# Optimization experiments

Hardware: AMD Instinct MI355X
Metric: run time of the kernel (lower is better)

The kernel has to match this reference:

```python
import jax, jax.numpy as jnp
import numpy as np

K_KNN = 20
TC = 3  # taylor_channel
N_TERMS = 20  # trivariate polynomial terms up to order 3
CHANNELS = [(6, 32), (32, 64), (64, 128), (128, 256)]


def _knn_indices(xyz, k):
    sq = jnp.sum(xyz * xyz, axis=1)  # B x N
    d2 = sq[:, :, None] + sq[:, None, :] - 2.0 * jnp.einsum('bci,bcj->bij', xyz, xyz)
    _, idx = jax.lax.top_k(-d2, k)
    return idx


def _group(feat, idx):
    # feat: B x C x N, idx: B x N x K -> B x C x N x K
    return jax.vmap(lambda f, i: f[:, i])(feat, idx)


def _taylor_terms(g):
    X, Y, Z = g[:, 0], g[:, 1], g[:, 2]
    one = jnp.ones_like(X)
    terms = [one, X, Y, Z, X * Y, X * Z, Y * Z, X * X, Y * Y, Z * Z,
             X * X * Y, X * X * Z, X * Y * Y, Y * Y * Z, X * Z * Z, Y * Z * Z,
             X * Y * Z, X * X * X, Y * Y * Y, Z * Z * Z]
    return jnp.stack(terms, axis=1)


def _spider_conv(feat, idx, terms, w1, b1, w2, b2):
    # feat: B x C x N; w1: tc x 20; w2: out x (C*tc) x K
    B, C, N = feat.shape
    g = _group(feat, idx)  # B x C x N x K
    taylor = jnp.einsum('btnk,ot->bonk', terms, w1) + b1[None, :, None, None]
    g = (g[:, :, None, :, :] * taylor[:, None, :, :, :]).reshape(B, C * TC, N, g.shape[-1])
    out = jnp.einsum('bcnk,ock->bon', g, w2) + b2[None, :, None]
    return jax.nn.relu(out)


def _forward(pc, params):
    # pc: B x N x 6
    pcT = jnp.transpose(pc, (0, 2, 1))
    xyz = pcT[:, 0:3, :]
    idx = _knn_indices(xyz, K_KNN)  # B x N x K
    grouped_xyz = _group(xyz, idx)
    grouped_pc = grouped_xyz - xyz[:, :, :, None]  # relative coords
    terms = _taylor_terms(grouped_pc)
    feat = pcT
    feats = []
    for l in range(4):
        w1, b1, w2, b2 = params[l]
        feat = _spider_conv(feat, idx, terms, w1, b1, w2, b2)
        feats.append(feat)
    cat = jnp.concatenate(feats, axis=1)
    top2, _ = jax.lax.top_k(cat, 2)  # topk over point dim (last axis)
    return top2.reshape(cat.shape[0], -1)  # B x 960


def setup_inputs() -> dict:
    key = jax.random.key(0)
    keys = jax.random.split(key, 1 + 16)
    B, N = 4, 2048
    inp = {'pc': jax.random.normal(keys[0], (B, N, 6), dtype=jnp.float32)}
    ki = 1
    for l, (cin, cout) in enumerate(CHANNELS):
        inp[f'w1_{l}'] = jax.random.normal(keys[ki], (TC, N_TERMS), dtype=jnp.float32) * 0.1; ki += 1
        inp[f'b1_{l}'] = jax.random.normal(keys[ki], (TC,), dtype=jnp.float32) * 0.01; ki += 1
        inp[f'w2_{l}'] = jax.random.normal(keys[ki], (cout, cin * TC, K_KNN), dtype=jnp.float32) * (1.0 / np.sqrt(cin * TC * K_KNN)); ki += 1
        inp[f'b2_{l}'] = jax.random.normal(keys[ki], (cout,), dtype=jnp.float32) * 0.01; ki += 1
    return inp


def reference(pc, w1_0, b1_0, w2_0, b2_0, w1_1, b1_1, w2_1, b2_1,
              w1_2, b1_2, w2_2, b2_2, w1_3, b1_3, w2_3, b2_3):
    params = [(w1_0, b1_0, w2_0, b2_0), (w1_1, b1_1, w2_1, b2_1),
              (w1_2, b1_2, w2_2, b2_2), (w1_3, b1_3, w2_3, b2_3)]
    return _forward(pc, params)
```

## Files before the change

kernel.cpp:

```cpp
#include <hip/hip_runtime.h>
#include <math.h>

#define BB 4
#define NN 2048
#define KNN 20

typedef _Float16 f16x8 __attribute__((ext_vector_type(8)));
typedef _Float16 f16x4 __attribute__((ext_vector_type(4)));
typedef _Float16 f16x2 __attribute__((ext_vector_type(2)));
typedef float f32x4 __attribute__((ext_vector_type(4)));

#define DPP_STEP(CTRL, RMASK)                                                   \
    {                                                                           \
        unsigned ov = (unsigned)__builtin_amdgcn_update_dpp(                    \
            (int)bv, (int)bv, CTRL, RMASK, 0xf, false);                         \
        unsigned oj = (unsigned)__builtin_amdgcn_update_dpp(                    \
            (int)jj, (int)jj, CTRL, RMASK, 0xf, false);                         \
        bool lt = (ov < bv) || (ov == bv && oj < jj);                           \
        bv = lt ? ov : bv;                                                      \
        jj = lt ? oj : jj;                                                      \
    }

__global__ __launch_bounds__(256) void knn_kernel(const float* __restrict__ pc,
                                                  int* __restrict__ idx_out,
                                                  float* __restrict__ rel_out) {
    __shared__ float4 sp[NN];
    const int tid = threadIdx.x;
    const int b = blockIdx.x / (NN / 4);
    const int grp = blockIdx.x % (NN / 4);
    for (int p = tid; p < NN; p += 256) {
        float x = pc[(size_t)(b * NN + p) * 6 + 0];
        float y = pc[(size_t)(b * NN + p) * 6 + 1];
        float z = pc[(size_t)(b * NN + p) * 6 + 2];
        float4 v;
        v.x = x; v.y = y; v.z = z;
        v.w = __fadd_rn(__fadd_rn(__fmul_rn(x, x), __fmul_rn(y, y)), __fmul_rn(z, z));
        sp[p] = v;
    }
    __syncthreads();
    const int lane = tid & 63;
    const int i = grp * 4 + (tid >> 6);
    const float4 pi = sp[i];
    const float xi = pi.x, yi = pi.y, zi = pi.z, sqi = pi.w;

    unsigned mmr[32];
#pragma unroll
    for (int t = 0; t < 32; ++t) {
        const int j = t * 64 + lane;
        const float4 pj = sp[j];
        float dot = __fadd_rn(__fadd_rn(__fmul_rn(xi, pj.x), __fmul_rn(yi, pj.y)),
                              __fmul_rn(zi, pj.z));
        float d2 = __fsub_rn(__fadd_rn(sqi, pj.w), __fmul_rn(2.0f, dot));
        unsigned bbits = __float_as_uint(d2);
        mmr[t] = bbits ^ (0x80000000u | (unsigned)((int)bbits >> 31));
    }

    const unsigned UMAX = 0xFFFFFFFFu;
    unsigned mask = 0u;
    unsigned v1, t1, v2, t2;

    auto refill = [&]() {
        v1 = UMAX; t1 = 0u; v2 = UMAX; t2 = 0u;
#pragma unroll
        for (int t = 0; t < 32; ++t) {
            unsigned m = ((mask >> t) & 1u) ? UMAX : mmr[t];
            bool c1 = m < v1;
            bool c2 = m < v2;
            unsigned nv2 = c1 ? v1 : (c2 ? m : v2);
            unsigned nt2 = c1 ? t1 : (c2 ? (unsigned)t : t2);
            v1 = c1 ? m : v1;
            t1 = c1 ? (unsigned)t : t1;
            v2 = nv2; t2 = nt2;
        }
    };
    refill();

    const size_t orow = (size_t)(b * NN + i);
    for (int k = 0; k < KNN; ++k) {
        unsigned bv = v1;
        unsigned jj = (t1 << 6) | (unsigned)lane;
        DPP_STEP(0x111, 0xf)
        DPP_STEP(0x112, 0xf)
        DPP_STEP(0x114, 0xf)
        DPP_STEP(0x118, 0xf)
        DPP_STEP(0x142, 0xa)
        DPP_STEP(0x143, 0xc)
        const unsigned sj = (unsigned)__builtin_amdgcn_readlane((int)jj, 63);
        if (lane == 0) {
            idx_out[orow * KNN + k] = (int)sj;
            const float4 pj = sp[sj];
            size_t ro = (orow * KNN + k) * 3;
            rel_out[ro + 0] = __fsub_rn(pj.x, xi);
            rel_out[ro + 1] = __fsub_rn(pj.y, yi);
            rel_out[ro + 2] = __fsub_rn(pj.z, zi);
        }
        if (k < KNN - 1) {
            bool am = ((sj & 63u) == (unsigned)lane);
            if (am) {
                mask |= (1u << (sj >> 6));
                v1 = v2; t1 = t2; v2 = UMAX;
            }
            if (__ballot(v1 == UMAX) != 0ull) refill();
        }
    }
}

__global__ __launch_bounds__(256) void taylor_all_kernel(
    const float* __restrict__ rel,
    const float* __restrict__ w10, const float* __restrict__ b10, _Float16* __restrict__ ty0,
    const float* __restrict__ w11, const float* __restrict__ b11, _Float16* __restrict__ ty1,
    const float* __restrict__ w12, const float* __restrict__ b12, _Float16* __restrict__ ty2,
    const float* __restrict__ w13, const float* __restrict__ b13, _Float16* __restrict__ ty3) {
    __shared__ float w1s[4][60];
    __shared__ float b1s[4][3];
    const int tid = threadIdx.x;
    if (tid < 240) {
        const float* wp = (tid < 60) ? w10 : (tid < 120) ? w11 : (tid < 180) ? w12 : w13;
        w1s[tid / 60][tid % 60] = wp[tid % 60];
    } else if (tid < 252) {
        int r = tid - 240;
        const float* bp = (r < 3) ? b10 : (r < 6) ? b11 : (r < 9) ? b12 : b13;
        b1s[r / 3][r % 3] = bp[r % 3];
    }
    __syncthreads();
    int t = blockIdx.x * 256 + tid;
    if (t >= BB * NN * KNN) return;
    float X = rel[(size_t)t * 3 + 0], Y = rel[(size_t)t * 3 + 1], Z = rel[(size_t)t * 3 + 2];
    float tm[20];
    tm[0] = 1.f; tm[1] = X; tm[2] = Y; tm[3] = Z;
    tm[4] = X * Y; tm[5] = X * Z; tm[6] = Y * Z;
    tm[7] = X * X; tm[8] = Y * Y; tm[9] = Z * Z;
    tm[10] = X * X * Y; tm[11] = X * X * Z; tm[12] = X * Y * Y; tm[13] = Y * Y * Z;
    tm[14] = X * Z * Z; tm[15] = Y * Z * Z; tm[16] = X * Y * Z;
    tm[17] = X * X * X; tm[18] = Y * Y * Y; tm[19] = Z * Z * Z;
    _Float16* typ[4] = {ty0, ty1, ty2, ty3};
#pragma unroll
    for (int l = 0; l < 4; ++l) {
#pragma unroll
        for (int o = 0; o < 3; ++o) {
            float a = b1s[l][o];
#pragma unroll
            for (int q = 0; q < 20; ++q) a += w1s[l][o * 20 + q] * tm[q];
            typ[l][(size_t)t * 3 + o] = (_Float16)a;
        }
    }
}

struct WsplitArgs {
    const float* w2[4];
    _Float16* wf[4];
    int COUT[4], CIN[4], CPAD[4], OCB[4], KCB[4];
    int cum[4];
};

__global__ __launch_bounds__(256) void wsplit_all_kernel(WsplitArgs a) {
    int e = blockIdx.x * 256 + threadIdx.x;
    if (e >= a.cum[3]) return;
    int l = (e >= a.cum[0]) + (e >= a.cum[1]) + (e >= a.cum[2]);
    int base = l ? a.cum[l - 1] : 0;
    e -= base;
    const int KCB = a.KCB[l], OCB = a.OCB[l], CPAD = a.CPAD[l], CIN = a.CIN[l];
    int i = e & 7;
    int lane = (e >> 3) & 63;
    int fi = e >> 9;
    int kcb = fi % KCB;
    int ocb = (fi / KCB) % OCB;
    int k = fi / (KCB * OCB);
    int oc = ocb * 16 + (lane & 15);
    int kk = kcb * 32 + (lane >> 4) * 8 + i;
    int o = kk / CPAD, c = kk % CPAD;
    float x = 0.f;
    if (o < 3 && c < CIN)
        x = a.w2[l][((size_t)oc * (CIN * 3) + c * 3 + o) * KNN + k];
    a.wf[l][e] = (_Float16)x;
}

template <int CIN, int COUT, int CK3P, int NT, int WM, int WN, int FM, int FN,
          int OCT, int KSPLIT, bool L0S, bool F16IN>
__global__ __launch_bounds__(256) void convm_kernel(const void* __restrict__ fin,
                                                    const int* __restrict__ idx,
                                                    const _Float16* __restrict__ tyg,
                                                    const _Float16* __restrict__ wf,
                                                    float* __restrict__ out) {
    constexpr int KR = KNN / KSPLIT;
    constexpr int SR = CK3P + 8;
    constexpr int KCB = CK3P / 32;
    constexpr int OCB = COUT / 16;
    constexpr int OCBLK = WM * FM * 16;
    constexpr int NTL = NN / NT;
    constexpr int TPR = 256 / NT;
    constexpr int CT = L0S ? 6 : (CIN / TPR);
    constexpr int CQ = L0S ? 2 : (CT >= 4 ? CT / 4 : 1);
    constexpr int GF = (CT >= 8) ? CT / 8 : 1;
    static_assert(WN * FN * 16 == NT, "n tiling");
    static_assert(OCBLK * OCT == COUT, "oc tiling");
    static_assert(WM * WN == 4, "4 waves");

    __shared__ _Float16 Bs[NT * SR];
    __shared__ _Float16 tyt[NT][3 * KR];
    __shared__ int idxt[NT][KR];

    const float* finf = (const float*)fin;
    const _Float16* finh = (const _Float16*)fin;

    const int tid = threadIdx.x;
    const int lane = tid & 63;
    const int wid = tid >> 6;
    const int wm = wid / WN;
    const int wn = wid % WN;
    int t = blockIdx.x;
    const int b = t % BB;      t /= BB;
    const int ks = t % KSPLIT; t /= KSPLIT;
    const int oct = t % OCT;   t /= OCT;
    const int ntl = t;
    const int n0 = ntl * NT;
    const int oc0 = oct * OCBLK;
    const int k0 = ks * KR;
    const size_t brow = (size_t)b * NN;

    for (int e = tid; e < NT * KR; e += 256) {
        int n = e / KR, kk = e % KR;
        idxt[n][kk] = idx[(brow + n0 + n) * KNN + k0 + kk];
    }
    for (int e = tid; e < NT * 3 * KR; e += 256) {
        int n = e / (3 * KR), q = e % (3 * KR);
        tyt[n][q] = tyg[((brow + n0 + n) * KNN + k0) * 3 + q];
    }
    __syncthreads();

    const int nrow = tid % NT;
    const int sub = tid / NT;
    float4 g[CQ];
    f16x8 gf[GF];

    auto issue_gather = [&](int kk) {
        if constexpr (L0S) {
            if (tid < 192) {
                int j = idxt[nrow][kk];
                const float* p = finf + (brow + j) * 6;
                g[0] = *reinterpret_cast<const float4*>(p);
                float2 r2 = *reinterpret_cast<const float2*>(p + 4);
                g[1].x = r2.x; g[1].y = r2.y;
            }
        } else if constexpr (F16IN) {
            int j = idxt[nrow][kk];
            const _Float16* p = finh + (brow + j) * CIN + sub * CT;
#pragma unroll
            for (int q = 0; q < GF; ++q)
                gf[q] = *reinterpret_cast<const f16x8*>(p + q * 8);
        } else {
            int j = idxt[nrow][kk];
            const float* p = finf + (brow + j) * CIN + sub * CT;
#pragma unroll
            for (int q = 0; q < CQ; ++q)
                g[q] = *reinterpret_cast<const float4*>(p + q * 4);
        }
    };
    issue_gather(0);

    f32x4 acc[FM][FN];
#pragma unroll
    for (int fm = 0; fm < FM; ++fm)
#pragma unroll
        for (int fn = 0; fn < FN; ++fn) acc[fm][fn] = (f32x4){0.f, 0.f, 0.f, 0.f};

    f16x8 areg[FM * KCB];
    auto loadA_burst = [&](int k) {
#pragma unroll
        for (int fm = 0; fm < FM; ++fm)
#pragma unroll
            for (int kcb = 0; kcb < KCB; ++kcb) {
                size_t fidx = ((size_t)k * OCB + (oc0 >> 4) + wm * FM + fm) * KCB + kcb;
                areg[fm * KCB + kcb] =
                    *reinterpret_cast<const f16x8*>(&wf[(fidx * 64 + lane) * 8]);
            }
    };

    for (int kk = 0; kk < KR; ++kk) {
        const int k = k0 + kk;
        loadA_burst(k);
        __syncthreads();
        if constexpr (L0S) {
            if (tid < 192) {
                _Float16 th = tyt[nrow][kk * 3 + sub];
                f16x2 tb; tb[0] = th; tb[1] = th;
                f16x2 g0, g1, g2;
                g0[0] = (_Float16)g[0].x; g0[1] = (_Float16)g[0].y;
                g1[0] = (_Float16)g[0].z; g1[1] = (_Float16)g[0].w;
                g2[0] = (_Float16)g[1].x; g2[1] = (_Float16)g[1].y;
                f16x2 p0 = g0 * tb, p1 = g1 * tb, p2 = g2 * tb;
                f16x8 hv;
                hv[0] = p0[0]; hv[1] = p0[1]; hv[2] = p1[0]; hv[3] = p1[1];
                hv[4] = p2[0]; hv[5] = p2[1]; hv[6] = (_Float16)0.f; hv[7] = (_Float16)0.f;
                *reinterpret_cast<f16x8*>(&Bs[nrow * SR + sub * 8]) = hv;
                if (sub == 0) {
                    f16x8 z = {};
                    *reinterpret_cast<f16x8*>(&Bs[nrow * SR + 24]) = z;
                }
            }
        } else {
            f16x2 gh[CT / 2];
            if constexpr (F16IN) {
                const f16x2* gp = reinterpret_cast<const f16x2*>(gf);
#pragma unroll
                for (int q = 0; q < CT / 2; ++q) gh[q] = gp[q];
            } else {
#pragma unroll
                for (int q = 0; q < CQ; ++q) {
                    f16x2 a0, a1;
                    a0[0] = (_Float16)g[q].x; a0[1] = (_Float16)g[q].y;
                    a1[0] = (_Float16)g[q].z; a1[1] = (_Float16)g[q].w;
                    gh[2 * q] = a0; gh[2 * q + 1] = a1;
                }
            }
            _Float16 th0 = tyt[nrow][kk * 3 + 0];
            _Float16 th1 = tyt[nrow][kk * 3 + 1];
            _Float16 th2 = tyt[nrow][kk * 3 + 2];
#pragma unroll
            for (int o = 0; o < 3; ++o) {
                _Float16 th = (o == 0) ? th0 : (o == 1) ? th1 : th2;
                f16x2 tb; tb[0] = th; tb[1] = th;
#pragma unroll
                for (int qp = 0; qp < CT / 8; ++qp) {
                    f16x2 p0 = gh[4 * qp + 0] * tb;
                    f16x2 p1 = gh[4 * qp + 1] * tb;
                    f16x2 p2 = gh[4 * qp + 2] * tb;
                    f16x2 p3 = gh[4 * qp + 3] * tb;
                    f16x8 hv;
                    hv[0] = p0[0]; hv[1] = p0[1]; hv[2] = p1[0]; hv[3] = p1[1];
                    hv[4] = p2[0]; hv[5] = p2[1]; hv[6] = p3[0]; hv[7] = p3[1];
                    *reinterpret_cast<f16x8*>(
                        &Bs[nrow * SR + o * CIN + sub * CT + qp * 8]) = hv;
                }
            }
        }
        __syncthreads();
        if (kk + 1 < KR) issue_gather(kk + 1);
#pragma unroll
        for (int kcb = 0; kcb < KCB; ++kcb) {
            f16x8 bf[FN];
#pragma unroll
            for (int fn = 0; fn < FN; ++fn) {
                int row = wn * FN * 16 + fn * 16 + (lane & 15);
                bf[fn] = *reinterpret_cast<const f16x8*>(
                    &Bs[row * SR + kcb * 32 + (lane >> 4) * 8]);
            }
#pragma unroll
            for (int fm = 0; fm < FM; ++fm)
#pragma unroll
                for (int fn = 0; fn < FN; ++fn)
                    acc[fm][fn] = __builtin_amdgcn_mfma_f32_16x16x32_f16(
                        areg[fm * KCB + kcb], bf[fn], acc[fm][fn], 0, 0, 0);
        }
    }
    float* dst = out + (size_t)ks * ((size_t)BB * NN * COUT);
#pragma unroll
    for (int fm = 0; fm < FM; ++fm) {
        const int ocb = oc0 + wm * FM * 16 + fm * 16 + ((lane >> 4) << 2);
#pragma unroll
        for (int fn = 0; fn < FN; ++fn) {
            int n = n0 + wn * FN * 16 + fn * 16 + (lane & 15);
            float4 o4;
            o4.x = acc[fm][fn][0]; o4.y = acc[fm][fn][1];
            o4.z = acc[fm][fn][2]; o4.w = acc[fm][fn][3];
            *reinterpret_cast<float4*>(&dst[(brow + n) * COUT + ocb]) = o4;
        }
    }
}

template <int CIN, int COUT, int CK3P, int NT, int WM, int WN, int FM, int FN,
          int OCT, int KSPLIT>
__global__ __launch_bounds__(256) void convp_kernel(const _Float16* __restrict__ fin,
                                                    const int* __restrict__ idx,
                                                    const _Float16* __restrict__ tyg,
                                                    const _Float16* __restrict__ wf,
                                                    float* __restrict__ out) {
    constexpr int KR = KNN / KSPLIT;
    constexpr int SR = CK3P + 8;
    constexpr int CKH = CK3P / 2;
    constexpr int KCB = CK3P / 32;
    constexpr int KCBH = KCB / 2;
    constexpr int OCB = COUT / 16;
    constexpr int OCBLK = WM * FM * 16;
    constexpr int NTL = NN / NT;
    constexpr int TPR = 256 / NT;
    constexpr int CT = CIN / TPR;
    constexpr int GF = CT / 8;
    static_assert(WN * FN * 16 == NT, "n tiling");
    static_assert(OCBLK * OCT == COUT, "oc tiling");
    static_assert(WM * WN == 4, "4 waves");

    __shared__ _Float16 Bs[NT * SR];
    __shared__ _Float16 tyt[NT][3 * KR];
    __shared__ int idxt[NT][KR];

    const int tid = threadIdx.x;
    const int lane = tid & 63;
    const int wid = tid >> 6;
    const int wm = wid / WN;
    const int wn = wid % WN;
    int t = blockIdx.x;
    const int b = t % BB;      t /= BB;
    const int ks = t % KSPLIT; t /= KSPLIT;
    const int oct = t % OCT;   t /= OCT;
    const int ntl = t;
    const int n0 = ntl * NT;
    const int oc0 = oct * OCBLK;
    const int k0 = ks * KR;
    const size_t brow = (size_t)b * NN;

    for (int e = tid; e < NT * KR; e += 256) {
        int n = e / KR, kk = e % KR;
        idxt[n][kk] = idx[(brow + n0 + n) * KNN + k0 + kk];
    }
    for (int e = tid; e < NT * 3 * KR; e += 256) {
        int n = e / (3 * KR), q = e % (3 * KR);
        tyt[n][q] = tyg[((brow + n0 + n) * KNN + k0) * 3 + q];
    }
    __syncthreads();

    const int nrow = tid % NT;
    const int sub = tid / NT;
    f16x8 gnext[GF];
    f16x2 ghc[CT / 2];

    auto issue_gather = [&](int kk) {
        int j = idxt[nrow][kk];
        const _Float16* p = fin + (brow + j) * CIN + sub * CT;
#pragma unroll
        for (int q = 0; q < GF; ++q)
            gnext[q] = *reinterpret_cast<const f16x8*>(p + q * 8);
    };
    auto commit_gh = [&]() {
        const f16x2* gp = reinterpret_cast<const f16x2*>(gnext);
#pragma unroll
        for (int q = 0; q < CT / 2; ++q) ghc[q] = gp[q];
    };
    auto buildB = [&](int h, int kk) {
        _Float16 th0 = tyt[nrow][kk * 3 + 0];
        _Float16 th1 = tyt[nrow][kk * 3 + 1];
        _Float16 th2 = tyt[nrow][kk * 3 + 2];
#pragma unroll
        for (int o = 0; o < 3; ++o) {
            const int kkpos = o * CIN + sub * CT;
            if (kkpos / CKH != h) continue;
            _Float16 th = (o == 0) ? th0 : (o == 1) ? th1 : th2;
            f16x2 tb; tb[0] = th; tb[1] = th;
#pragma unroll
            for (int qp = 0; qp < CT / 8; ++qp) {
                f16x2 p0 = ghc[4 * qp + 0] * tb;
                f16x2 p1 = ghc[4 * qp + 1] * tb;
                f16x2 p2 = ghc[4 * qp + 2] * tb;
                f16x2 p3 = ghc[4 * qp + 3] * tb;
                f16x8 hv;
                hv[0] = p0[0]; hv[1] = p0[1]; hv[2] = p1[0]; hv[3] = p1[1];
                hv[4] = p2[0]; hv[5] = p2[1]; hv[6] = p3[0]; hv[7] = p3[1];
                *reinterpret_cast<f16x8*>(&Bs[nrow * SR + kkpos + qp * 8]) = hv;
            }
        }
    };

    f32x4 acc[FM][FN];
#pragma unroll
    for (int fm = 0; fm < FM; ++fm)
#pragma unroll
        for (int fn = 0; fn < FN; ++fn) acc[fm][fn] = (f32x4){0.f, 0.f, 0.f, 0.f};

    f16x8 regA[FM * KCBH], regB[FM * KCBH];
    auto loadA = [&](int k, int h, f16x8* dst) {
#pragma unroll
        for (int fm = 0; fm < FM; ++fm)
#pragma unroll
            for (int kcb = 0; kcb < KCBH; ++kcb) {
                size_t fidx = ((size_t)k * OCB + (oc0 >> 4) + wm * FM + fm) * KCB +
                              h * KCBH + kcb;
                dst[fm * KCBH + kcb] =
                    *reinterpret_cast<const f16x8*>(&wf[(fidx * 64 + lane) * 8]);
            }
    };
    auto mfma_half = [&](int h, const f16x8* areg) {
#pragma unroll
        for (int kcb = 0; kcb < KCBH; ++kcb) {
            const int kabs = h * KCBH + kcb;
            f16x8 bf[FN];
#pragma unroll
            for (int fn = 0; fn < FN; ++fn) {
                int row = wn * FN * 16 + fn * 16 + (lane & 15);
                bf[fn] = *reinterpret_cast<const f16x8*>(
                    &Bs[row * SR + kabs * 32 + (lane >> 4) * 8]);
            }
#pragma unroll
            for (int fm = 0; fm < FM; ++fm)
#pragma unroll
                for (int fn = 0; fn < FN; ++fn)
                    acc[fm][fn] = __builtin_amdgcn_mfma_f32_16x16x32_f16(
                        areg[fm * KCBH + kcb], bf[fn], acc[fm][fn], 0, 0, 0);
        }
    };

    issue_gather(0);
    commit_gh();
    loadA(k0, 0, regA);
    buildB(0, 0);
    __syncthreads();

    for (int kk = 0; kk < KR; ++kk) {
        const int k = k0 + kk;
        loadA(k, 1, regB);
        if (kk + 1 < KR) issue_gather(kk + 1);
        buildB(1, kk);
        mfma_half(0, regA);
        __syncthreads();
        if (kk + 1 < KR) {
            loadA(k + 1, 0, regA);
            commit_gh();
            buildB(0, kk + 1);
        }
        mfma_half(1, regB);
        __syncthreads();
    }

    float* dst = out + (size_t)ks * ((size_t)BB * NN * COUT);
#pragma unroll
    for (int fm = 0; fm < FM; ++fm) {
        const int ocb = oc0 + wm * FM * 16 + fm * 16 + ((lane >> 4) << 2);
#pragma unroll
        for (int fn = 0; fn < FN; ++fn) {
            int n = n0 + wn * FN * 16 + fn * 16 + (lane & 15);
            float4 o4;
            o4.x = acc[fm][fn][0]; o4.y = acc[fm][fn][1];
            o4.z = acc[fm][fn][2]; o4.w = acc[fm][fn][3];
            *reinterpret_cast<float4*>(&dst[(brow + n) * COUT + ocb]) = o4;
        }
    }
}

template <int COUT, int KS>
__global__ __launch_bounds__(256) void combine_kernel(const float* __restrict__ p,
                                                      const float* __restrict__ b2,
                                                      _Float16* __restrict__ out) {
    constexpr size_t TOT = (size_t)BB * NN * COUT;
    size_t i = (size_t)blockIdx.x * 256 + threadIdx.x;
    if (i * 4 >= TOT) return;
    const float4* p4 = reinterpret_cast<const float4*>(p);
    float4 a = p4[i];
#pragma unroll
    for (int s = 1; s < KS; ++s) {
        float4 v = p4[i + s * (TOT / 4)];
        a.x += v.x; a.y += v.y; a.z += v.z; a.w += v.w;
    }
    float4 bb = *reinterpret_cast<const float4*>(&b2[(i * 4) % COUT]);
    f16x4 r;
    r[0] = (_Float16)fmaxf(a.x + bb.x, 0.f);
    r[1] = (_Float16)fmaxf(a.y + bb.y, 0.f);
    r[2] = (_Float16)fmaxf(a.z + bb.z, 0.f);
    r[3] = (_Float16)fmaxf(a.w + bb.w, 0.f);
    *reinterpret_cast<f16x4*>(&out[i * 4]) = r;
}

__global__ __launch_bounds__(256) void top2_kernel(const _Float16* __restrict__ f1,
                                                   const _Float16* __restrict__ f2,
                                                   const _Float16* __restrict__ f3,
                                                   const float* __restrict__ p3,
                                                   const float* __restrict__ b23,
                                                   float* __restrict__ out) {
    __shared__ float m1s[256], m2s[256];
    const int bid = blockIdx.x;
    const int b = bid / 480;
    const int ch = bid % 480;
    const size_t brow = (size_t)b * NN;
    float m1 = -INFINITY, m2 = -INFINITY;
    if (ch < 224) {
        const _Float16* f; int C, c;
        if (ch < 32)       { f = f1; C = 32;  c = ch; }
        else if (ch < 96)  { f = f2; C = 64;  c = ch - 32; }
        else               { f = f3; C = 128; c = ch - 96; }
        for (int n = threadIdx.x; n < NN; n += 256) {
            float v = (float)f[(brow + n) * C + c];
            if (v > m1) { m2 = m1; m1 = v; }
            else if (v > m2) m2 = v;
        }
    } else {
        const int c = ch - 224;
        const float bc = b23[c];
        constexpr size_t TOT3 = (size_t)BB * NN * 256;
        for (int n = threadIdx.x; n < NN; n += 256) {
            size_t o = (brow + n) * 256 + c;
            float v = fmaxf(p3[o] + p3[TOT3 + o] + bc, 0.f);
            if (v > m1) { m2 = m1; m1 = v; }
            else if (v > m2) m2 = v;
        }
    }
    m1s[threadIdx.x] = m1; m2s[threadIdx.x] = m2;
    __syncthreads();
    for (int s = 128; s > 0; s >>= 1) {
        if (threadIdx.x < s) {
            float a1 = m1s[threadIdx.x], a2 = m2s[threadIdx.x];
            float c1 = m1s[threadIdx.x + s], c2 = m2s[threadIdx.x + s];
            m1s[threadIdx.x] = fmaxf(a1, c1);
            m2s[threadIdx.x] = fmaxf(fminf(a1, c1), fmaxf(a2, c2));
        }
        __syncthreads();
    }
    if (threadIdx.x == 0) {
        out[(size_t)b * 960 + ch * 2 + 0] = m1s[0];
        out[(size_t)b * 960 + ch * 2 + 1] = m2s[0];
    }
}

extern "C" void kernel_launch(void* const* d_in, const int* in_sizes, int n_in,
                              void* d_out, int out_size, void* d_ws, size_t ws_size,
                              hipStream_t stream) {
    const float* pc = (const float*)d_in[0];
    const float *w1[4], *b1[4], *w2[4], *b2[4];
    for (int l = 0; l < 4; ++l) {
        w1[l] = (const float*)d_in[1 + 4 * l];
        b1[l] = (const float*)d_in[2 + 4 * l];
        w2[l] = (const float*)d_in[3 + 4 * l];
        b2[l] = (const float*)d_in[4 + 4 * l];
    }
    char* ws = (char*)d_ws;
    size_t off = 0;
    auto alloc = [&](size_t bytes) -> void* {
        void* p = ws + off;
        off = (off + bytes + 255) & ~(size_t)255;
        return p;
    };
    int* idxb      = (int*)alloc((size_t)BB * NN * KNN * 4);
    float* rel     = (float*)alloc((size_t)BB * NN * KNN * 3 * 4);
    _Float16* ty0  = (_Float16*)alloc((size_t)BB * NN * KNN * 3 * 2);
    _Float16* ty1  = (_Float16*)alloc((size_t)BB * NN * KNN * 3 * 2);
    _Float16* ty2  = (_Float16*)alloc((size_t)BB * NN * KNN * 3 * 2);
    _Float16* ty3  = (_Float16*)alloc((size_t)BB * NN * KNN * 3 * 2);
    const int wtot0 = KNN * 2 * 1 * 512;
    const int wtot1 = KNN * 4 * 3 * 512;
    const int wtot2 = KNN * 8 * 6 * 512;
    const int wtot3 = KNN * 16 * 12 * 512;
    _Float16* wf0 = (_Float16*)alloc((size_t)wtot0 * 2);
    _Float16* wf1 = (_Float16*)alloc((size_t)wtot1 * 2);
    _Float16* wf2 = (_Float16*)alloc((size_t)wtot2 * 2);
    _Float16* wf3 = (_Float16*)alloc((size_t)wtot3 * 2);
    _Float16* f1  = (_Float16*)alloc((size_t)BB * NN * 32 * 2);
    _Float16* f2  = (_Float16*)alloc((size_t)BB * NN * 64 * 2);
    _Float16* f3  = (_Float16*)alloc((size_t)BB * NN * 128 * 2);
    float* pbuf   = (float*)alloc((size_t)4 * BB * NN * 128 * 4);

    knn_kernel<<<BB * NN / 4, 256, 0, stream>>>(pc, idxb, rel);

    taylor_all_kernel<<<(BB * NN * KNN + 255) / 256, 256, 0, stream>>>(
        rel, w1[0], b1[0], ty0, w1[1], b1[1], ty1, w1[2], b1[2], ty2, w1[3], b1[3], ty3);

    WsplitArgs wa;
    wa.w2[0] = w2[0]; wa.w2[1] = w2[1]; wa.w2[2] = w2[2]; wa.w2[3] = w2[3];
    wa.wf[0] = wf0; wa.wf[1] = wf1; wa.wf[2] = wf2; wa.wf[3] = wf3;
    int COUTs[4] = {32, 64, 128, 256}, CINs[4] = {6, 32, 64, 128};
    int CPADs[4] = {8, 32, 64, 128}, OCBs[4] = {2, 4, 8, 16}, KCBs[4] = {1, 3, 6, 12};
    int cum = 0;
    for (int l = 0; l < 4; ++l) {
        wa.COUT[l] = COUTs[l]; wa.CIN[l] = CINs[l]; wa.CPAD[l] = CPADs[l];
        wa.OCB[l] = OCBs[l]; wa.KCB[l] = KCBs[l];
        cum += KNN * OCBs[l] * KCBs[l] * 512;
        wa.cum[l] = cum;
    }
    wsplit_all_kernel<<<(cum + 255) / 256, 256, 0, stream>>>(wa);

    convm_kernel<6, 32, 32, 64, 2, 2, 1, 2, 1, 4, true, false>
        <<<512, 256, 0, stream>>>(pc, idxb, ty0, wf0, pbuf);
    combine_kernel<32, 4><<<(BB * NN * 32 / 4 + 255) / 256, 256, 0, stream>>>(pbuf, b2[0], f1);

    convm_kernel<32, 64, 96, 64, 4, 1, 1, 4, 1, 4, false, true>
        <<<512, 256, 0, stream>>>(f1, idxb, ty1, wf1, pbuf);
    combine_kernel<64, 4><<<(BB * NN * 64 / 4 + 255) / 256, 256, 0, stream>>>(pbuf, b2[1], f2);

    convp_kernel<64, 128, 192, 64, 4, 1, 2, 4, 1, 4>
        <<<512, 256, 0, stream>>>(f2, idxb, ty2, wf2, pbuf);
    combine_kernel<128, 4><<<(BB * NN * 128 / 4 + 255) / 256, 256, 0, stream>>>(pbuf, b2[2], f3);

    convp_kernel<128, 256, 384, 64, 4, 1, 2, 4, 2, 2>
        <<<512, 256, 0, stream>>>(f3, idxb, ty3, wf3, pbuf);

    top2_kernel<<<BB * 480, 256, 0, stream>>>(f1, f2, f3, pbuf, b2[3], (float*)d_out);
}
```

Measured before the change: 174.8 us.

## Switch layer 2-3 conv to 32x32x16 MFMA with register-held indices

Rewrites the layer 2 and 3 gather-conv kernel to use 32x32x16 f16 MFMA tiles instead of 16x16x32. Each wave now owns 32 output channels across all 64 points, and the weight pre-split kernel gets a matching 32-row fragment layout. Neighbor indices and Taylor coefficients are loaded straight into registers rather than staged through shared memory, which removes one barrier and some LDS traffic. The cost is more register pressure from the fully unrolled k loop and the per-thread index and coefficient arrays.

```diff
diff --git a/kernel.cpp b/kernel.cpp
--- a/kernel.cpp
+++ b/kernel.cpp
@@ -9,6 +9,7 @@
 typedef _Float16 f16x4 __attribute__((ext_vector_type(4)));
 typedef _Float16 f16x2 __attribute__((ext_vector_type(2)));
 typedef float f32x4 __attribute__((ext_vector_type(4)));
+typedef float f32x16 __attribute__((ext_vector_type(16)));
 
 #define DPP_STEP(CTRL, RMASK)                                                   \
     {                                                                           \
@@ -149,7 +150,7 @@
 struct WsplitArgs {
     const float* w2[4];
     _Float16* wf[4];
-    int COUT[4], CIN[4], CPAD[4], OCB[4], KCB[4];
+    int CIN[4], CPAD[4], OCB[4], KCB[4], M32[4];
     int cum[4];
 };
 
@@ -166,8 +167,14 @@
     int kcb = fi % KCB;
     int ocb = (fi / KCB) % OCB;
     int k = fi / (KCB * OCB);
-    int oc = ocb * 16 + (lane & 15);
-    int kk = kcb * 32 + (lane >> 4) * 8 + i;
+    int oc, kk;
+    if (a.M32[l]) {
+        oc = ocb * 32 + (lane & 31);
+        kk = kcb * 16 + (lane >> 5) * 8 + i;
+    } else {
+        oc = ocb * 16 + (lane & 15);
+        kk = kcb * 32 + (lane >> 4) * 8 + i;
+    }
     int o = kk / CPAD, c = kk % CPAD;
     float x = 0.f;
     if (o < 3 && c < CIN)
@@ -368,37 +375,31 @@
     }
 }
 
-template <int CIN, int COUT, int CK3P, int NT, int WM, int WN, int FM, int FN,
-          int OCT, int KSPLIT>
-__global__ __launch_bounds__(256) void convp_kernel(const _Float16* __restrict__ fin,
-                                                    const int* __restrict__ idx,
-                                                    const _Float16* __restrict__ tyg,
-                                                    const _Float16* __restrict__ wf,
-                                                    float* __restrict__ out) {
+template <int CIN, int COUT, int CK3P, int OCT, int KSPLIT>
+__global__ __launch_bounds__(256) void convp32_kernel(const _Float16* __restrict__ fin,
+                                                      const int* __restrict__ idx,
+                                                      const _Float16* __restrict__ tyg,
+                                                      const _Float16* __restrict__ wf,
+                                                      float* __restrict__ out) {
+    constexpr int NT = 64;
     constexpr int KR = KNN / KSPLIT;
     constexpr int SR = CK3P + 8;
     constexpr int CKH = CK3P / 2;
-    constexpr int KCB = CK3P / 32;
-    constexpr int KCBH = KCB / 2;
-    constexpr int OCB = COUT / 16;
-    constexpr int OCBLK = WM * FM * 16;
+    constexpr int KC16 = CK3P / 16;
+    constexpr int KC16H = KC16 / 2;
+    constexpr int OCB32 = COUT / 32;
+    constexpr int OCBLK = 128;
     constexpr int NTL = NN / NT;
-    constexpr int TPR = 256 / NT;
-    constexpr int CT = CIN / TPR;
+    constexpr int CT = CIN / 4;
     constexpr int GF = CT / 8;
-    static_assert(WN * FN * 16 == NT, "n tiling");
     static_assert(OCBLK * OCT == COUT, "oc tiling");
-    static_assert(WM * WN == 4, "4 waves");
+    static_assert(CKH % 16 == 0, "half alignment");
 
     __shared__ _Float16 Bs[NT * SR];
-    __shared__ _Float16 tyt[NT][3 * KR];
-    __shared__ int idxt[NT][KR];
 
     const int tid = threadIdx.x;
     const int lane = tid & 63;
-    const int wid = tid >> 6;
-    const int wm = wid / WN;
-    const int wn = wid % WN;
+    const int wm = tid >> 6;
     int t = blockIdx.x;
     const int b = t % BB;      t /= BB;
     const int ks = t % KSPLIT; t /= KSPLIT;
@@ -409,37 +410,52 @@
     const int k0 = ks * KR;
     const size_t brow = (size_t)b * NN;
 
-    for (int e = tid; e < NT * KR; e += 256) {
-        int n = e / KR, kk = e % KR;
-        idxt[n][kk] = idx[(brow + n0 + n) * KNN + k0 + kk];
-    }
-    for (int e = tid; e < NT * 3 * KR; e += 256) {
-        int n = e / (3 * KR), q = e % (3 * KR);
-        tyt[n][q] = tyg[((brow + n0 + n) * KNN + k0) * 3 + q];
-    }
-    __syncthreads();
-
     const int nrow = tid % NT;
     const int sub = tid / NT;
+
+    int idxr[KR];
+    _Float16 tyr[3 * KR];
+    {
+        const int* ip = &idx[(brow + n0 + nrow) * KNN + k0];
+#pragma unroll
+        for (int kk = 0; kk < KR; ++kk) idxr[kk] = ip[kk];
+        const _Float16* tp = &tyg[((brow + n0 + nrow) * KNN + k0) * 3];
+#pragma unroll
+        for (int q = 0; q < 3 * KR; ++q) tyr[q] = tp[q];
+    }
+
     f16x8 gnext[GF];
     f16x2 ghc[CT / 2];
 
-    auto issue_gather = [&](int kk) {
-        int j = idxt[nrow][kk];
-        const _Float16* p = fin + (brow + j) * CIN + sub * CT;
-#pragma unroll
-        for (int q = 0; q < GF; ++q)
-            gnext[q] = *reinterpret_cast<const f16x8*>(p + q * 8);
+    f32x16 acc[2];
+#pragma unroll
+    for (int nh = 0; nh < 2; ++nh)
+#pragma unroll
+        for (int q = 0; q < 16; ++q) acc[nh][q] = 0.f;
+
+    f16x8 regA[KC16H], regB[KC16H];
+    auto loadA = [&](int k, int h, f16x8* dst) {
+#pragma unroll
+        for (int kcb = 0; kcb < KC16H; ++kcb) {
+            size_t fidx = ((size_t)k * OCB32 + (oc0 >> 5) + wm) * KC16 + h * KC16H + kcb;
+            dst[kcb] = *reinterpret_cast<const f16x8*>(&wf[(fidx * 64 + lane) * 8]);
+        }
     };
-    auto commit_gh = [&]() {
-        const f16x2* gp = reinterpret_cast<const f16x2*>(gnext);
-#pragma unroll
-        for (int q = 0; q < CT / 2; ++q) ghc[q] = gp[q];
+    auto mfma_half = [&](int h, const f16x8* areg) {
+#pragma unroll
+        for (int kcb = 0; kcb < KC16H; ++kcb) {
+            const int kabs = h * KC16H + kcb;
+#pragma unroll
+            for (int nh = 0; nh < 2; ++nh) {
+                int row = nh * 32 + (lane & 31);
+                f16x8 bf = *reinterpret_cast<const f16x8*>(
+                    &Bs[row * SR + kabs * 16 + (lane >> 5) * 8]);
+                acc[nh] = __builtin_amdgcn_mfma_f32_32x32x16_f16(
+                    areg[kcb], bf, acc[nh], 0, 0, 0);
+            }
+        }
     };
-    auto buildB = [&](int h, int kk) {
-        _Float16 th0 = tyt[nrow][kk * 3 + 0];
-        _Float16 th1 = tyt[nrow][kk * 3 + 1];
-        _Float16 th2 = tyt[nrow][kk * 3 + 2];
+    auto buildB = [&](int h, _Float16 th0, _Float16 th1, _Float16 th2) {
 #pragma unroll
         for (int o = 0; o < 3; ++o) {
             const int kkpos = o * CIN + sub * CT;
@@ -460,77 +476,57 @@
         }
     };
 
-    f32x4 acc[FM][FN];
-#pragma unroll
-    for (int fm = 0; fm < FM; ++fm)
-#pragma unroll
-        for (int fn = 0; fn < FN; ++fn) acc[fm][fn] = (f32x4){0.f, 0.f, 0.f, 0.f};
-
-    f16x8 regA[FM * KCBH], regB[FM * KCBH];
-    auto loadA = [&](int k, int h, f16x8* dst) {
-#pragma unroll
-        for (int fm = 0; fm < FM; ++fm)
-#pragma unroll
-            for (int kcb = 0; kcb < KCBH; ++kcb) {
-                size_t fidx = ((size_t)k * OCB + (oc0 >> 4) + wm * FM + fm) * KCB +
-                              h * KCBH + kcb;
-                dst[fm * KCBH + kcb] =
-                    *reinterpret_cast<const f16x8*>(&wf[(fidx * 64 + lane) * 8]);
-            }
-    };
-    auto mfma_half = [&](int h, const f16x8* areg) {
-#pragma unroll
-        for (int kcb = 0; kcb < KCBH; ++kcb) {
-            const int kabs = h * KCBH + kcb;
-            f16x8 bf[FN];
-#pragma unroll
-            for (int fn = 0; fn < FN; ++fn) {
-                int row = wn * FN * 16 + fn * 16 + (lane & 15);
-                bf[fn] = *reinterpret_cast<const f16x8*>(
-                    &Bs[row * SR + kabs * 32 + (lane >> 4) * 8]);
-            }
-#pragma unroll
-            for (int fm = 0; fm < FM; ++fm)
-#pragma unroll
-                for (int fn = 0; fn < FN; ++fn)
-                    acc[fm][fn] = __builtin_amdgcn_mfma_f32_16x16x32_f16(
-                        areg[fm * KCBH + kcb], bf[fn], acc[fm][fn], 0, 0, 0);
-        }
-    };
-
-    issue_gather(0);
-    commit_gh();
+    {
+        const _Float16* p = fin + (brow + idxr[0]) * CIN + sub * CT;
+#pragma unroll
+        for (int q = 0; q < GF; ++q)
+            gnext[q] = *reinterpret_cast<const f16x8*>(p + q * 8);
+        const f16x2* gp = reinterpret_cast<const f16x2*>(gnext);
+#pragma unroll
+        for (int q = 0; q < CT / 2; ++q) ghc[q] = gp[q];
+    }
     loadA(k0, 0, regA);
-    buildB(0, 0);
+    buildB(0, tyr[0], tyr[1], tyr[2]);
     __syncthreads();
 
+#pragma unroll
     for (int kk = 0; kk < KR; ++kk) {
         const int k = k0 + kk;
         loadA(k, 1, regB);
-        if (kk + 1 < KR) issue_gather(kk + 1);
-        buildB(1, kk);
+        if (kk + 1 < KR) {
+            const _Float16* p = fin + (brow + idxr[kk + 1]) * CIN + sub * CT;
+#pragma unroll
+            for (int q = 0; q < GF; ++q)
+                gnext[q] = *reinterpret_cast<const f16x8*>(p + q * 8);
+        }
+        buildB(1, tyr[kk * 3 + 0], tyr[kk * 3 + 1], tyr[kk * 3 + 2]);
         mfma_half(0, regA);
         __syncthreads();
         if (kk + 1 < KR) {
             loadA(k + 1, 0, regA);
-            commit_gh();
-            buildB(0, kk + 1);
+            const f16x2* gp = reinterpret_cast<const f16x2*>(gnext);
+#pragma unroll
+            for (int q = 0; q < CT / 2; ++q) ghc[q] = gp[q];
+            buildB(0, tyr[(kk + 1) * 3 + 0], tyr[(kk + 1) * 3 + 1], tyr[(kk + 1) * 3 + 2]);
         }
         mfma_half(1, regB);
         __syncthreads();
     }
 
     float* dst = out + (size_t)ks * ((size_t)BB * NN * COUT);
-#pragma unroll
-    for (int fm = 0; fm < FM; ++fm) {
-        const int ocb = oc0 + wm * FM * 16 + fm * 16 + ((lane >> 4) << 2);
-#pragma unroll
-        for (int fn = 0; fn < FN; ++fn) {
-            int n = n0 + wn * FN * 16 + fn * 16 + (lane & 15);
+    const int ocw = oc0 + wm * 32;
+    const int hi4 = ((lane >> 5) << 2);
+#pragma unroll
+    for (int nh = 0; nh < 2; ++nh) {
+        int n = n0 + nh * 32 + (lane & 31);
+#pragma unroll
+        for (int j = 0; j < 4; ++j) {
             float4 o4;
-            o4.x = acc[fm][fn][0]; o4.y = acc[fm][fn][1];
-            o4.z = acc[fm][fn][2]; o4.w = acc[fm][fn][3];
-            *reinterpret_cast<float4*>(&dst[(brow + n) * COUT + ocb]) = o4;
+            o4.x = acc[nh][4 * j + 0];
+            o4.y = acc[nh][4 * j + 1];
+            o4.z = acc[nh][4 * j + 2];
+            o4.w = acc[nh][4 * j + 3];
+            *reinterpret_cast<float4*>(&dst[(brow + n) * COUT + ocw + j * 8 + hi4]) = o4;
         }
     }
 }
@@ -634,8 +630,8 @@
     _Float16* ty3  = (_Float16*)alloc((size_t)BB * NN * KNN * 3 * 2);
     const int wtot0 = KNN * 2 * 1 * 512;
     const int wtot1 = KNN * 4 * 3 * 512;
-    const int wtot2 = KNN * 8 * 6 * 512;
-    const int wtot3 = KNN * 16 * 12 * 512;
+    const int wtot2 = KNN * 4 * 12 * 512;
+    const int wtot3 = KNN * 8 * 24 * 512;
     _Float16* wf0 = (_Float16*)alloc((size_t)wtot0 * 2);
     _Float16* wf1 = (_Float16*)alloc((size_t)wtot1 * 2);
     _Float16* wf2 = (_Float16*)alloc((size_t)wtot2 * 2);
@@ -653,12 +649,15 @@
     WsplitArgs wa;
     wa.w2[0] = w2[0]; wa.w2[1] = w2[1]; wa.w2[2] = w2[2]; wa.w2[3] = w2[3];
     wa.wf[0] = wf0; wa.wf[1] = wf1; wa.wf[2] = wf2; wa.wf[3] = wf3;
-    int COUTs[4] = {32, 64, 128, 256}, CINs[4] = {6, 32, 64, 128};
-    int CPADs[4] = {8, 32, 64, 128}, OCBs[4] = {2, 4, 8, 16}, KCBs[4] = {1, 3, 6, 12};
+    int CINs[4] = {6, 32, 64, 128};
+    int CPADs[4] = {8, 32, 64, 128};
+    int OCBs[4] = {2, 4, 4, 8};
+    int KCBs[4] = {1, 3, 12, 24};
+    int M32s[4] = {0, 0, 1, 1};
     int cum = 0;
     for (int l = 0; l < 4; ++l) {
-        wa.COUT[l] = COUTs[l]; wa.CIN[l] = CINs[l]; wa.CPAD[l] = CPADs[l];
-        wa.OCB[l] = OCBs[l]; wa.KCB[l] = KCBs[l];
+        wa.CIN[l] = CINs[l]; wa.CPAD[l] = CPADs[l];
+        wa.OCB[l] = OCBs[l]; wa.KCB[l] = KCBs[l]; wa.M32[l] = M32s[l];
         cum += KNN * OCBs[l] * KCBs[l] * 512;
         wa.cum[l] = cum;
     }
@@ -672,11 +671,11 @@
         <<<512, 256, 0, stream>>>(f1, idxb, ty1, wf1, pbuf);
     combine_kernel<64, 4><<<(BB * NN * 64 / 4 + 255) / 256, 256, 0, stream>>>(pbuf, b2[1], f2);
 
-    convp_kernel<64, 128, 192, 64, 4, 1, 2, 4, 1, 4>
+    convp32_kernel<64, 128, 192, 1, 4>
         <<<512, 256, 0, stream>>>(f2, idxb, ty2, wf2, pbuf);
     combine_kernel<128, 4><<<(BB * NN * 128 / 4 + 255) / 256, 256, 0, stream>>>(pbuf, b2[2], f3);
 
-    convp_kernel<128, 256, 384, 64, 4, 1, 2, 4, 2, 2>
+    convp32_kernel<128, 256, 384, 2, 2>
         <<<512, 256, 0, stream>>>(f3, idxb, ty3, wf3, pbuf);
 
     top2_kernel<<<BB * 480, 256, 0, stream>>>(f1, f2, f3, pbuf, b2[3], (float*)d_out);
```

After: 169.8 us. 2.9% less time.
